# Kernel optimization log

Measured on AMD Instinct MI355X. Metric: run time of the kernel, lower is better.

The kernel has to match this reference:

```python
import jax, jax.numpy as jnp
import numpy as np

TEMPERATURE = 0.1


def setup_inputs() -> dict:
    key = jax.random.key(0)
    k1, k2 = jax.random.split(key)
    N, D = 8192, 128
    feature_embeds = jax.random.normal(k1, (N, D), dtype=jnp.float32)
    label_ids = jax.random.randint(k2, (N,), 0, 33, dtype=jnp.int64)
    return {"feature_embeds": feature_embeds, "label_ids": label_ids}


def reference(feature_embeds, label_ids):
    # L2-normalize embeddings (original applies F.normalize twice; idempotent)
    x = feature_embeds / jnp.linalg.norm(feature_embeds, axis=-1, keepdims=True)

    N = x.shape[0]
    # pairwise similarity logits [N, N]
    logits = (x @ x.T) / TEMPERATURE

    same = (label_ids[:, None] == label_ids[None, :]).astype(x.dtype)
    eye = jnp.eye(N, dtype=x.dtype)
    numerator_mask = same * (1.0 - eye)      # positives, excluding self
    denominator_mask = 1.0 - eye             # all others, excluding self

    e = jnp.exp(logits)
    Z = jnp.sum(e * denominator_mask, axis=-1)           # [N]
    # log(exp(logits)/Z) = logits - log Z
    log_prob = logits - jnp.log(Z)[:, None]

    pos_count = jnp.sum(numerator_mask, axis=-1)         # [N]
    valid = pos_count > 0
    per_row = jnp.sum(log_prob * numerator_mask, axis=-1) / jnp.where(valid, pos_count, 1.0)
    per_row = jnp.where(valid, per_row, 0.0)
    n_valid = jnp.sum(valid.astype(x.dtype))
    loss = -jnp.sum(per_row) / n_valid
    return loss
```

## Files before the change

### kernel.cpp

```cpp
#include <hip/hip_runtime.h>
#include <math.h>

#define NN 8192
#define DD 128
#define JR 16
#define JW (NN / JR)
#define KE 14.42695040888963f

typedef __attribute__((ext_vector_type(8))) short short8;
typedef __attribute__((ext_vector_type(4))) float f32x4;

__device__ __forceinline__ unsigned short f2bf(float f) {
    unsigned u = __builtin_bit_cast(unsigned, f);
    unsigned r = (u + 0x7FFFu + ((u >> 16) & 1u)) >> 16;
    return (unsigned short)r;
}
__device__ __forceinline__ float bf2f(unsigned short h) {
    unsigned u = ((unsigned)h) << 16;
    return __builtin_bit_cast(float, u);
}

__global__ __launch_bounds__(256) void prep_kernel(const float* __restrict__ x,
                                                   unsigned short* __restrict__ xn,
                                                   float* __restrict__ sd) {
    int row  = (blockIdx.x << 2) + (threadIdx.x >> 6);
    int lane = threadIdx.x & 63;
    float2 v = ((const float2*)(x + (size_t)row * DD))[lane];
    float ss = v.x * v.x + v.y * v.y;
    #pragma unroll
    for (int off = 32; off; off >>= 1) ss += __shfl_xor(ss, off);
    float rn = rsqrtf(ss);
    unsigned short bx = f2bf(v.x * rn), by = f2bf(v.y * rn);
    ushort2 st; st.x = bx; st.y = by;
    ((ushort2*)(xn + (size_t)row * DD))[lane] = st;
    float fx = bf2f(bx), fy = bf2f(by);
    float s2 = fx * fx + fy * fy;
    #pragma unroll
    for (int off = 32; off; off >>= 1) s2 += __shfl_xor(s2, off);
    if (lane == 0) sd[row] = s2;
}

__global__ __launch_bounds__(256, 2) void cl_main(const unsigned short* __restrict__ xn,
                                                  const int* __restrict__ labels,
                                                  float* __restrict__ Zp,
                                                  float* __restrict__ Sp) {
    const int tid  = threadIdx.x;
    const int wi   = tid >> 6;
    const int lane = tid & 63;
    const int l15  = lane & 15;
    const int lhi  = lane >> 4;
    const int b    = (int)blockIdx.x;
    const int jrange = b & 15;
    const int strip  = ((b >> 4) << 2) | wi;
    const int row0   = strip << 6;

    short8 a[4][4];
    #pragma unroll
    for (int mi = 0; mi < 4; ++mi)
        #pragma unroll
        for (int ks = 0; ks < 4; ++ks)
            a[mi][ks] = *(const short8*)(xn + (size_t)(row0 + mi * 16 + l15) * DD + ks * 32 + lhi * 8);

    int labI[4][4];
    #pragma unroll
    for (int mi = 0; mi < 4; ++mi)
        #pragma unroll
        for (int r = 0; r < 4; ++r)
            labI[mi][r] = labels[row0 + mi * 16 + lhi * 4 + r];

    float z[4][4], s[4][4];
    #pragma unroll
    for (int mi = 0; mi < 4; ++mi)
        #pragma unroll
        for (int r = 0; r < 4; ++r) { z[mi][r] = 0.f; s[mi][r] = 0.f; }

    const int j0r = jrange * JW;
    for (int t = 0; t < JW / 64; ++t) {
        const int j0 = j0r + t * 64;
        int lj[4];
        #pragma unroll
        for (int ni = 0; ni < 4; ++ni) lj[ni] = labels[j0 + ni * 16 + l15];

        f32x4 acc[4][4];
        #pragma unroll
        for (int mi = 0; mi < 4; ++mi)
            #pragma unroll
            for (int ni = 0; ni < 4; ++ni) acc[mi][ni] = (f32x4){0.f, 0.f, 0.f, 0.f};

        #pragma unroll
        for (int ni = 0; ni < 4; ++ni) {
            short8 bf[4];
            #pragma unroll
            for (int ks = 0; ks < 4; ++ks)
                bf[ks] = *(const short8*)(xn + (size_t)(j0 + ni * 16 + l15) * DD + ks * 32 + lhi * 8);
            #pragma unroll
            for (int ks = 0; ks < 4; ++ks)
                #pragma unroll
                for (int mi = 0; mi < 4; ++mi)
                    acc[mi][ni] = __builtin_amdgcn_mfma_f32_16x16x32_bf16(a[mi][ks], bf[ks], acc[mi][ni], 0, 0, 0);
        }

        #pragma unroll
        for (int mi = 0; mi < 4; ++mi)
            #pragma unroll
            for (int ni = 0; ni < 4; ++ni)
                #pragma unroll
                for (int r = 0; r < 4; ++r) {
                    float d = acc[mi][ni][r];
                    z[mi][r] += __builtin_amdgcn_exp2f(d * KE);
                    s[mi][r] += (lj[ni] == labI[mi][r]) ? d : 0.f;
                }
    }

    #pragma unroll
    for (int mi = 0; mi < 4; ++mi)
        #pragma unroll
        for (int r = 0; r < 4; ++r) {
            float zz = z[mi][r], ss = s[mi][r];
            #pragma unroll
            for (int off = 1; off < 16; off <<= 1) {
                zz += __shfl_xor(zz, off);
                ss += __shfl_xor(ss, off);
            }
            if (l15 == 0) {
                int row = row0 + mi * 16 + lhi * 4 + r;
                Zp[jrange * NN + row] = zz;
                Sp[jrange * NN + row] = ss;
            }
        }
}

__global__ __launch_bounds__(256) void fin1(const float* __restrict__ Zp,
                                            const float* __restrict__ Sp,
                                            const float* __restrict__ sd,
                                            const int* __restrict__ labels,
                                            float* __restrict__ psum,
                                            float* __restrict__ pcnt) {
    __shared__ int cnt[33];
    __shared__ float rs[4], rc[4];
    int t = threadIdx.x;
    if (t < 33) cnt[t] = 0;
    __syncthreads();
    for (int i = t; i < NN; i += 256) atomicAdd(&cnt[labels[i]], 1);
    __syncthreads();

    int row = blockIdx.x * 256 + t;
    float Z = 0.f, S = 0.f;
    #pragma unroll
    for (int jr = 0; jr < JR; ++jr) {
        Z += Zp[jr * NN + row];
        S += Sp[jr * NN + row];
    }
    float sv = sd[row];
    Z -= __builtin_amdgcn_exp2f(sv * KE);
    S -= sv;
    int C = cnt[labels[row]] - 1;
    float pr = 0.f, vl = 0.f;
    if (C > 0) { pr = 10.f * S / (float)C - logf(Z); vl = 1.f; }
    #pragma unroll
    for (int off = 32; off; off >>= 1) { pr += __shfl_xor(pr, off); vl += __shfl_xor(vl, off); }
    int wv = t >> 6, ln = t & 63;
    if (ln == 0) { rs[wv] = pr; rc[wv] = vl; }
    __syncthreads();
    if (t == 0) {
        psum[blockIdx.x] = rs[0] + rs[1] + rs[2] + rs[3];
        pcnt[blockIdx.x] = rc[0] + rc[1] + rc[2] + rc[3];
    }
}

__global__ void fin2(const float* __restrict__ psum, const float* __restrict__ pcnt,
                     float* __restrict__ out) {
    int t = threadIdx.x;
    float a = t < 32 ? psum[t] : 0.f;
    float c = t < 32 ? pcnt[t] : 0.f;
    #pragma unroll
    for (int off = 32; off; off >>= 1) { a += __shfl_xor(a, off); c += __shfl_xor(c, off); }
    if (t == 0) out[0] = -a / c;
}

extern "C" void kernel_launch(void* const* d_in, const int* in_sizes, int n_in,
                              void* d_out, int out_size, void* d_ws, size_t ws_size,
                              hipStream_t stream) {
    const float* x      = (const float*)d_in[0];
    const int*   labels = (const int*)d_in[1];
    float* out = (float*)d_out;
    char*  ws  = (char*)d_ws;

    unsigned short* xn = (unsigned short*)ws;
    float* sd   = (float*)(ws + 2097152);
    float* Zp   = (float*)(ws + 2097152 + 32768);
    float* Sp   = (float*)(ws + 2097152 + 32768 + 524288);
    float* psum = (float*)(ws + 2097152 + 32768 + 2 * 524288);
    float* pcnt = (float*)(ws + 2097152 + 32768 + 2 * 524288 + 128);

    prep_kernel<<<NN / 4, 256, 0, stream>>>(x, xn, sd);
    cl_main<<<(NN / 64 / 4) * JR, 256, 0, stream>>>(xn, labels, Zp, Sp);
    fin1<<<NN / 256, 256, 0, stream>>>(Zp, Sp, sd, labels, psum, pcnt);
    fin2<<<1, 64, 0, stream>>>(psum, pcnt, out);
}
```

Before: 112.3 us.

## Compute positive-pair sums via per-class embedding sums instead of masked pairwise accumulation

Rewrites the positive-logit sum as a dot product between each row and the sum of embeddings sharing its label. Two new kernels build those per-class sums and label counts, so the main pairwise kernel only accumulates the exp-based denominator with no label comparisons. The main kernel also switches to 32-row strips per wave with a higher occupancy hint, doubling the block count. This adds two small launches and an unnecessary __syncthreads in the hot loop. The class sums use bf16-rounded embeddings accumulated in fp32, so summation order changes slightly.

New measurement: 146.7 us. 30.7% more time.

```diff
diff --git a/kernel.cpp b/kernel.cpp
--- a/kernel.cpp
+++ b/kernel.cpp
@@ -4,8 +4,8 @@
 #define NN 8192
 #define DD 128
 #define JR 16
-#define JW (NN / JR)
 #define KE 14.42695040888963f
+#define NCLS 33
 
 typedef __attribute__((ext_vector_type(8))) short short8;
 typedef __attribute__((ext_vector_type(4))) float f32x4;
@@ -40,50 +40,81 @@
     if (lane == 0) sd[row] = s2;
 }
 
-__global__ __launch_bounds__(256, 2) void cl_main(const unsigned short* __restrict__ xn,
-                                                  const int* __restrict__ labels,
-                                                  float* __restrict__ Zp,
-                                                  float* __restrict__ Sp) {
+__global__ __launch_bounds__(256) void gsum_kernel(const unsigned short* __restrict__ xn,
+                                                   const int* __restrict__ labels,
+                                                   float* __restrict__ Gpart,
+                                                   int* __restrict__ cntpart) {
+    __shared__ float Gl[2][NCLS][DD];
+    __shared__ int   ch[NCLS];
+    const int t = threadIdx.x;
+    const int rbase = blockIdx.x * 128;
+    for (int i = t; i < 2 * NCLS * DD; i += 256) ((float*)Gl)[i] = 0.f;
+    if (t < NCLS) ch[t] = 0;
+    __syncthreads();
+    if (t < 128) atomicAdd(&ch[labels[rbase + t]], 1);
+    const int g = t >> 7, f = t & 127;
+    #pragma unroll 4
+    for (int k = 0; k < 64; ++k) {
+        int r = rbase + g * 64 + k;
+        int c = labels[r];
+        Gl[g][c][f] += bf2f(xn[(size_t)r * DD + f]);
+    }
+    __syncthreads();
+    for (int i = t; i < NCLS * DD; i += 256)
+        Gpart[(size_t)blockIdx.x * (NCLS * DD) + i] = ((float*)Gl)[i] + ((float*)Gl)[NCLS * DD + i];
+    if (t < NCLS) cntpart[blockIdx.x * NCLS + t] = ch[t];
+}
+
+__global__ __launch_bounds__(128) void greduce_kernel(const float* __restrict__ Gpart,
+                                                      const int* __restrict__ cntpart,
+                                                      float* __restrict__ G,
+                                                      int* __restrict__ cnt) {
+    const int c = blockIdx.x, f = threadIdx.x;
+    float s = 0.f;
+    #pragma unroll 8
+    for (int k = 0; k < 64; ++k) s += Gpart[(size_t)k * (NCLS * DD) + c * DD + f];
+    G[c * DD + f] = s;
+    if (f == 0) {
+        int s2 = 0;
+        for (int k = 0; k < 64; ++k) s2 += cntpart[k * NCLS + c];
+        cnt[c] = s2;
+    }
+}
+
+__global__ __launch_bounds__(256, 4) void cl_main(const unsigned short* __restrict__ xn,
+                                                  float* __restrict__ Zp) {
     const int tid  = threadIdx.x;
     const int wi   = tid >> 6;
     const int lane = tid & 63;
     const int l15  = lane & 15;
     const int lhi  = lane >> 4;
     const int b    = (int)blockIdx.x;
-    const int jrange = b & 15;
-    const int strip  = ((b >> 4) << 2) | wi;
-    const int row0   = strip << 6;
-
-    short8 a[4][4];
-    #pragma unroll
-    for (int mi = 0; mi < 4; ++mi)
+    const int jr   = b & (JR - 1);
+    const int sg   = b >> 4;
+    const int strip = sg * 4 + wi;
+    const int row0  = strip * 32;
+
+    short8 a[2][4];
+    #pragma unroll
+    for (int mi = 0; mi < 2; ++mi)
         #pragma unroll
         for (int ks = 0; ks < 4; ++ks)
             a[mi][ks] = *(const short8*)(xn + (size_t)(row0 + mi * 16 + l15) * DD + ks * 32 + lhi * 8);
 
-    int labI[4][4];
-    #pragma unroll
-    for (int mi = 0; mi < 4; ++mi)
-        #pragma unroll
-        for (int r = 0; r < 4; ++r)
-            labI[mi][r] = labels[row0 + mi * 16 + lhi * 4 + r];
-
-    float z[4][4], s[4][4];
-    #pragma unroll
-    for (int mi = 0; mi < 4; ++mi)
-        #pragma unroll
-        for (int r = 0; r < 4; ++r) { z[mi][r] = 0.f; s[mi][r] = 0.f; }
-
-    const int j0r = jrange * JW;
-    for (int t = 0; t < JW / 64; ++t) {
-        const int j0 = j0r + t * 64;
-        int lj[4];
-        #pragma unroll
-        for (int ni = 0; ni < 4; ++ni) lj[ni] = labels[j0 + ni * 16 + l15];
-
-        f32x4 acc[4][4];
-        #pragma unroll
-        for (int mi = 0; mi < 4; ++mi)
+    float z[2][4];
+    #pragma unroll
+    for (int mi = 0; mi < 2; ++mi)
+        #pragma unroll
+        for (int r = 0; r < 4; ++r) z[mi][r] = 0.f;
+
+    const int j0r = jr * (NN / JR);
+    for (int t8 = 0; t8 < (NN / JR) / 64; ++t8) {
+        __syncthreads();
+        const int j0 = j0r + t8 * 64;
+
+        f32x4 acc[2][4];
+        #pragma unroll
+        for (int mi = 0; mi < 2; ++mi)
             #pragma unroll
             for (int ni = 0; ni < 4; ++ni) acc[mi][ni] = (f32x4){0.f, 0.f, 0.f, 0.f};
 
@@ -96,65 +127,62 @@
             #pragma unroll
             for (int ks = 0; ks < 4; ++ks)
                 #pragma unroll
-                for (int mi = 0; mi < 4; ++mi)
+                for (int mi = 0; mi < 2; ++mi)
                     acc[mi][ni] = __builtin_amdgcn_mfma_f32_16x16x32_bf16(a[mi][ks], bf[ks], acc[mi][ni], 0, 0, 0);
         }
 
         #pragma unroll
-        for (int mi = 0; mi < 4; ++mi)
+        for (int mi = 0; mi < 2; ++mi)
             #pragma unroll
             for (int ni = 0; ni < 4; ++ni)
                 #pragma unroll
-                for (int r = 0; r < 4; ++r) {
-                    float d = acc[mi][ni][r];
-                    z[mi][r] += __builtin_amdgcn_exp2f(d * KE);
-                    s[mi][r] += (lj[ni] == labI[mi][r]) ? d : 0.f;
-                }
-    }
-
-    #pragma unroll
-    for (int mi = 0; mi < 4; ++mi)
+                for (int r = 0; r < 4; ++r)
+                    z[mi][r] += __builtin_amdgcn_exp2f(acc[mi][ni][r] * KE);
+    }
+
+    #pragma unroll
+    for (int mi = 0; mi < 2; ++mi)
         #pragma unroll
         for (int r = 0; r < 4; ++r) {
-            float zz = z[mi][r], ss = s[mi][r];
-            #pragma unroll
-            for (int off = 1; off < 16; off <<= 1) {
-                zz += __shfl_xor(zz, off);
-                ss += __shfl_xor(ss, off);
-            }
-            if (l15 == 0) {
-                int row = row0 + mi * 16 + lhi * 4 + r;
-                Zp[jrange * NN + row] = zz;
-                Sp[jrange * NN + row] = ss;
-            }
+            float zz = z[mi][r];
+            #pragma unroll
+            for (int off = 1; off < 16; off <<= 1) zz += __shfl_xor(zz, off);
+            if (l15 == 0)
+                Zp[(size_t)jr * NN + row0 + mi * 16 + lhi * 4 + r] = zz;
         }
 }
 
 __global__ __launch_bounds__(256) void fin1(const float* __restrict__ Zp,
-                                            const float* __restrict__ Sp,
+                                            const unsigned short* __restrict__ xn,
+                                            const float* __restrict__ G,
+                                            const int* __restrict__ cnt,
                                             const float* __restrict__ sd,
                                             const int* __restrict__ labels,
                                             float* __restrict__ psum,
                                             float* __restrict__ pcnt) {
-    __shared__ int cnt[33];
     __shared__ float rs[4], rc[4];
-    int t = threadIdx.x;
-    if (t < 33) cnt[t] = 0;
-    __syncthreads();
-    for (int i = t; i < NN; i += 256) atomicAdd(&cnt[labels[i]], 1);
-    __syncthreads();
-
-    int row = blockIdx.x * 256 + t;
-    float Z = 0.f, S = 0.f;
-    #pragma unroll
-    for (int jr = 0; jr < JR; ++jr) {
-        Z += Zp[jr * NN + row];
-        S += Sp[jr * NN + row];
-    }
+    const int t = threadIdx.x;
+    const int row = blockIdx.x * 256 + t;
+
+    float Z = 0.f;
+    #pragma unroll
+    for (int jr = 0; jr < JR; ++jr) Z += Zp[(size_t)jr * NN + row];
     float sv = sd[row];
     Z -= __builtin_amdgcn_exp2f(sv * KE);
+
+    const int c = labels[row];
+    const float* gc = G + c * DD;
+    float S = 0.f;
+    #pragma unroll 4
+    for (int k = 0; k < DD / 8; ++k) {
+        short8 v = *(const short8*)(xn + (size_t)row * DD + k * 8);
+        #pragma unroll
+        for (int e = 0; e < 8; ++e)
+            S = fmaf(bf2f((unsigned short)v[e]), gc[k * 8 + e], S);
+    }
     S -= sv;
-    int C = cnt[labels[row]] - 1;
+
+    int C = cnt[c] - 1;
     float pr = 0.f, vl = 0.f;
     if (C > 0) { pr = 10.f * S / (float)C - logf(Z); vl = 1.f; }
     #pragma unroll
@@ -186,15 +214,21 @@
     float* out = (float*)d_out;
     char*  ws  = (char*)d_ws;
 
-    unsigned short* xn = (unsigned short*)ws;
-    float* sd   = (float*)(ws + 2097152);
-    float* Zp   = (float*)(ws + 2097152 + 32768);
-    float* Sp   = (float*)(ws + 2097152 + 32768 + 524288);
-    float* psum = (float*)(ws + 2097152 + 32768 + 2 * 524288);
-    float* pcnt = (float*)(ws + 2097152 + 32768 + 2 * 524288 + 128);
+    size_t off = 0;
+    unsigned short* xn = (unsigned short*)(ws + off); off += (size_t)NN * DD * 2;
+    float* sd      = (float*)(ws + off); off += (size_t)NN * 4;
+    float* Zp      = (float*)(ws + off); off += (size_t)JR * NN * 4;
+    float* Gpart   = (float*)(ws + off); off += (size_t)64 * NCLS * DD * 4;
+    int*   cntpart = (int*)(ws + off);   off += (size_t)64 * NCLS * 4;
+    float* G       = (float*)(ws + off); off += (size_t)NCLS * DD * 4;
+    int*   cnt     = (int*)(ws + off);   off += 256;
+    float* psum    = (float*)(ws + off); off += 128;
+    float* pcnt    = (float*)(ws + off); off += 128;
 
     prep_kernel<<<NN / 4, 256, 0, stream>>>(x, xn, sd);
-    cl_main<<<(NN / 64 / 4) * JR, 256, 0, stream>>>(xn, labels, Zp, Sp);
-    fin1<<<NN / 256, 256, 0, stream>>>(Zp, Sp, sd, labels, psum, pcnt);
+    gsum_kernel<<<64, 256, 0, stream>>>(xn, labels, Gpart, cntpart);
+    greduce_kernel<<<NCLS, 128, 0, stream>>>(Gpart, cntpart, G, cnt);
+    cl_main<<<64 * JR, 256, 0, stream>>>(xn, Zp);
+    fin1<<<NN / 256, 256, 0, stream>>>(Zp, xn, G, cnt, sd, labels, psum, pcnt);
     fin2<<<1, 64, 0, stream>>>(psum, pcnt, out);
 }
```

## Stage B tiles in double-buffered swizzled LDS and fold temperature into embeddings

Applied to the files above, without the earlier changes.

The main kernel now uses 512-thread blocks (8 waves sharing one column range) and stages each 64-row B tile cooperatively into a double-buffered, XOR-swizzled LDS buffer. This replaces per-wave global loads of the same B data, and the next tile is prefetched while MFMAs run. The temperature scale is folded into the bf16 normalized embeddings, which removes a multiply before each exp2; fin1 rescales by ln2 to compensate. Per-row partials are now combined with atomicAdd into zeroed buffers instead of 16 strided partial arrays, at the cost of atomics, nondeterministic summation order, and extra bf16 rounding from the scaled values.

Result: faster. 91.03 us (-18.9%).

```diff
diff --git a/kernel.cpp b/kernel.cpp
--- a/kernel.cpp
+++ b/kernel.cpp
@@ -4,8 +4,10 @@
 #define NN 8192
 #define DD 128
 #define JR 16
-#define JW (NN / JR)
-#define KE 14.42695040888963f
+#define NT ((NN / JR) / 64)
+#define SQKE 3.7982825f
+#define LN2 0.6931471805599453f
+#define NCLS 33
 
 typedef __attribute__((ext_vector_type(8))) short short8;
 typedef __attribute__((ext_vector_type(4))) float f32x4;
@@ -22,15 +24,20 @@
 
 __global__ __launch_bounds__(256) void prep_kernel(const float* __restrict__ x,
                                                    unsigned short* __restrict__ xn,
-                                                   float* __restrict__ sd) {
-    int row  = (blockIdx.x << 2) + (threadIdx.x >> 6);
-    int lane = threadIdx.x & 63;
+                                                   float* __restrict__ sd,
+                                                   float* __restrict__ zs) {
+    const int b = blockIdx.x, t = threadIdx.x;
+    const int zi = b * 256 + t;
+    if (zi < 2 * NN + 64) zs[zi] = 0.f;
+
+    int row  = (b << 2) + (t >> 6);
+    int lane = t & 63;
     float2 v = ((const float2*)(x + (size_t)row * DD))[lane];
     float ss = v.x * v.x + v.y * v.y;
     #pragma unroll
     for (int off = 32; off; off >>= 1) ss += __shfl_xor(ss, off);
-    float rn = rsqrtf(ss);
-    unsigned short bx = f2bf(v.x * rn), by = f2bf(v.y * rn);
+    float rs = rsqrtf(ss) * SQKE;
+    unsigned short bx = f2bf(v.x * rs), by = f2bf(v.y * rs);
     ushort2 st; st.x = bx; st.y = by;
     ((ushort2*)(xn + (size_t)row * DD))[lane] = st;
     float fx = bf2f(bx), fy = bf2f(by);
@@ -40,19 +47,22 @@
     if (lane == 0) sd[row] = s2;
 }
 
-__global__ __launch_bounds__(256, 2) void cl_main(const unsigned short* __restrict__ xn,
+__global__ __launch_bounds__(512, 2) void cl_main(const unsigned short* __restrict__ xn,
                                                   const int* __restrict__ labels,
-                                                  float* __restrict__ Zp,
-                                                  float* __restrict__ Sp) {
+                                                  float* __restrict__ Z,
+                                                  float* __restrict__ S) {
+    __shared__ __align__(16) unsigned short Bt[2][64][DD];
+
     const int tid  = threadIdx.x;
-    const int wi   = tid >> 6;
+    const int w    = tid >> 6;
     const int lane = tid & 63;
     const int l15  = lane & 15;
     const int lhi  = lane >> 4;
     const int b    = (int)blockIdx.x;
-    const int jrange = b & 15;
-    const int strip  = ((b >> 4) << 2) | wi;
-    const int row0   = strip << 6;
+    const int jr   = b & (JR - 1);
+    const int panel = b >> 4;
+    const int row0  = panel * 512 + w * 64;
+    const int j0r   = jr * (NN / JR);
 
     short8 a[4][4];
     #pragma unroll
@@ -68,19 +78,41 @@
         for (int r = 0; r < 4; ++r)
             labI[mi][r] = labels[row0 + mi * 16 + lhi * 4 + r];
 
+    const int r4 = lane >> 4, kk = lane & 15;
+    const int srow0 = w * 8 + r4;
+    const int srow1 = w * 8 + 4 + r4;
+    const unsigned short* sg0 = xn + (size_t)(j0r + srow0) * DD + (kk ^ (srow0 & 7)) * 8;
+    const unsigned short* sg1 = xn + (size_t)(j0r + srow1) * DD + (kk ^ (srow1 & 7)) * 8;
+
     float z[4][4], s[4][4];
     #pragma unroll
     for (int mi = 0; mi < 4; ++mi)
         #pragma unroll
         for (int r = 0; r < 4; ++r) { z[mi][r] = 0.f; s[mi][r] = 0.f; }
 
-    const int j0r = jrange * JW;
-    for (int t = 0; t < JW / 64; ++t) {
-        const int j0 = j0r + t * 64;
+    {
+        short8 t0 = *(const short8*)sg0;
+        short8 t1 = *(const short8*)sg1;
+        *(short8*)&Bt[0][srow0][kk * 8] = t0;
+        *(short8*)&Bt[0][srow1][kk * 8] = t1;
+    }
+    __syncthreads();
+
+    const int sw = l15 & 7;
+    int cur = 0;
+    for (int t8 = 0; t8 < NT; ++t8) {
+        const int j0 = j0r + t8 * 64;
+
+        short8 nx0, nx1;
+        if (t8 < NT - 1) {
+            nx0 = *(const short8*)(sg0 + (size_t)(t8 + 1) * 64 * DD);
+            nx1 = *(const short8*)(sg1 + (size_t)(t8 + 1) * 64 * DD);
+        }
         int lj[4];
         #pragma unroll
         for (int ni = 0; ni < 4; ++ni) lj[ni] = labels[j0 + ni * 16 + l15];
 
+        const char* rbase = (const char*)&Bt[cur][0][0] + l15 * 256;
         f32x4 acc[4][4];
         #pragma unroll
         for (int mi = 0; mi < 4; ++mi)
@@ -89,15 +121,15 @@
 
         #pragma unroll
         for (int ni = 0; ni < 4; ++ni) {
-            short8 bf[4];
+            short8 bfv[4];
             #pragma unroll
             for (int ks = 0; ks < 4; ++ks)
-                bf[ks] = *(const short8*)(xn + (size_t)(j0 + ni * 16 + l15) * DD + ks * 32 + lhi * 8);
+                bfv[ks] = *(const short8*)(rbase + ni * 4096 + ((((ks << 2) | lhi) ^ sw) << 4));
             #pragma unroll
             for (int ks = 0; ks < 4; ++ks)
                 #pragma unroll
                 for (int mi = 0; mi < 4; ++mi)
-                    acc[mi][ni] = __builtin_amdgcn_mfma_f32_16x16x32_bf16(a[mi][ks], bf[ks], acc[mi][ni], 0, 0, 0);
+                    acc[mi][ni] = __builtin_amdgcn_mfma_f32_16x16x32_bf16(a[mi][ks], bfv[ks], acc[mi][ni], 0, 0, 0);
         }
 
         #pragma unroll
@@ -107,9 +139,16 @@
                 #pragma unroll
                 for (int r = 0; r < 4; ++r) {
                     float d = acc[mi][ni][r];
-                    z[mi][r] += __builtin_amdgcn_exp2f(d * KE);
+                    z[mi][r] += __builtin_amdgcn_exp2f(d);
                     s[mi][r] += (lj[ni] == labI[mi][r]) ? d : 0.f;
                 }
+
+        if (t8 < NT - 1) {
+            *(short8*)&Bt[cur ^ 1][srow0][kk * 8] = nx0;
+            *(short8*)&Bt[cur ^ 1][srow1][kk * 8] = nx1;
+        }
+        __syncthreads();
+        cur ^= 1;
     }
 
     #pragma unroll
@@ -124,39 +163,32 @@
             }
             if (l15 == 0) {
                 int row = row0 + mi * 16 + lhi * 4 + r;
-                Zp[jrange * NN + row] = zz;
-                Sp[jrange * NN + row] = ss;
+                atomicAdd(&Z[row], zz);
+                atomicAdd(&S[row], ss);
             }
         }
 }
 
-__global__ __launch_bounds__(256) void fin1(const float* __restrict__ Zp,
-                                            const float* __restrict__ Sp,
+__global__ __launch_bounds__(256) void fin1(const float* __restrict__ Z,
+                                            const float* __restrict__ S,
                                             const float* __restrict__ sd,
                                             const int* __restrict__ labels,
                                             float* __restrict__ psum,
                                             float* __restrict__ pcnt) {
-    __shared__ int cnt[33];
+    __shared__ int cnt[NCLS];
     __shared__ float rs[4], rc[4];
-    int t = threadIdx.x;
-    if (t < 33) cnt[t] = 0;
+    const int t = threadIdx.x;
+    if (t < NCLS) cnt[t] = 0;
     __syncthreads();
     for (int i = t; i < NN; i += 256) atomicAdd(&cnt[labels[i]], 1);
     __syncthreads();
 
-    int row = blockIdx.x * 256 + t;
-    float Z = 0.f, S = 0.f;
-    #pragma unroll
-    for (int jr = 0; jr < JR; ++jr) {
-        Z += Zp[jr * NN + row];
-        S += Sp[jr * NN + row];
-    }
-    float sv = sd[row];
-    Z -= __builtin_amdgcn_exp2f(sv * KE);
-    S -= sv;
+    const int row = blockIdx.x * 256 + t;
+    float Zr = Z[row] - __builtin_amdgcn_exp2f(sd[row]);
+    float Sr = S[row] - sd[row];
     int C = cnt[labels[row]] - 1;
     float pr = 0.f, vl = 0.f;
-    if (C > 0) { pr = 10.f * S / (float)C - logf(Z); vl = 1.f; }
+    if (C > 0) { pr = LN2 * Sr / (float)C - logf(Zr); vl = 1.f; }
     #pragma unroll
     for (int off = 32; off; off >>= 1) { pr += __shfl_xor(pr, off); vl += __shfl_xor(vl, off); }
     int wv = t >> 6, ln = t & 63;
@@ -186,15 +218,17 @@
     float* out = (float*)d_out;
     char*  ws  = (char*)d_ws;
 
-    unsigned short* xn = (unsigned short*)ws;
-    float* sd   = (float*)(ws + 2097152);
-    float* Zp   = (float*)(ws + 2097152 + 32768);
-    float* Sp   = (float*)(ws + 2097152 + 32768 + 524288);
-    float* psum = (float*)(ws + 2097152 + 32768 + 2 * 524288);
-    float* pcnt = (float*)(ws + 2097152 + 32768 + 2 * 524288 + 128);
-
-    prep_kernel<<<NN / 4, 256, 0, stream>>>(x, xn, sd);
-    cl_main<<<(NN / 64 / 4) * JR, 256, 0, stream>>>(xn, labels, Zp, Sp);
-    fin1<<<NN / 256, 256, 0, stream>>>(Zp, Sp, sd, labels, psum, pcnt);
+    size_t off = 0;
+    unsigned short* xn = (unsigned short*)(ws + off); off += (size_t)NN * DD * 2;
+    float* sd = (float*)(ws + off); off += (size_t)NN * 4;
+    float* zs = (float*)(ws + off); off += (size_t)(2 * NN + 64) * 4;
+    float* Z    = zs;
+    float* S    = zs + NN;
+    float* psum = zs + 2 * NN;
+    float* pcnt = zs + 2 * NN + 32;
+
+    prep_kernel<<<NN / 4, 256, 0, stream>>>(x, xn, sd, zs);
+    cl_main<<<(NN / 512) * JR, 512, 0, stream>>>(xn, labels, Z, S);
+    fin1<<<NN / 256, 256, 0, stream>>>(Z, S, sd, labels, psum, pcnt);
     fin2<<<1, 64, 0, stream>>>(psum, pcnt, out);
 }
```
